# Kernel optimization log

Measured on AMD Instinct MI355X. Metric: run time of the kernel, lower is better.

## Reference

```python
import jax, jax.numpy as jnp
import numpy as np

B, N, XD = 64, 512, 32  # batch, n_points, x_dims (feature columns); last 2 cols are t, y


def setup_inputs() -> dict:
    key = jax.random.key(0)
    xtys = jax.random.normal(key, (B, N, XD + 2), dtype=jnp.float32)
    return {"xtys": xtys}


def _linear_dml(xtys):
    b, n, D = xtys.shape
    d = D - 2
    xs = xtys[..., :d]          # (b, n, d) covariates
    ts = xtys[..., d]           # (b, n)   treatment
    ys = xtys[..., d + 1]       # (b, n)   outcome

    # Growing-prefix least squares via cumulative sufficient statistics.
    # For prefix i (rows 0..i): min-norm lstsq solution w = pinv(X^T X) X^T v == pinv(X) v,
    # matching torch.linalg.lstsq (gelsy/gelsd) semantics including rank-deficient prefixes.
    G = jnp.cumsum(jnp.einsum('bnd,bne->bnde', xs, xs), axis=1)      # (b,n,d,d) Gram
    Xty = jnp.cumsum(xs * ys[..., None], axis=1)                     # (b,n,d)
    Xtt = jnp.cumsum(xs * ts[..., None], axis=1)                     # (b,n,d)
    Sty = jnp.cumsum(ts * ys, axis=1)                                # (b,n)
    Stt = jnp.cumsum(ts * ts, axis=1)                                # (b,n)

    Ginv = jnp.linalg.pinv(G)                                        # batched pinv, (b,n,d,d)
    wy = jnp.einsum('bnde,bne->bnd', Ginv, Xty)
    wt = jnp.einsum('bnde,bne->bnd', Ginv, Xtt)

    # ate_i = <t_res, y_res> / <t_res, t_res> over prefix, expanded via the stats above.
    num = (Sty
           - jnp.einsum('bnd,bnd->bn', wt, Xty)
           - jnp.einsum('bnd,bnd->bn', wy, Xtt)
           + jnp.einsum('bnd,bnde,bne->bn', wt, G, wy))
    den = (Stt
           - 2.0 * jnp.einsum('bnd,bnd->bn', wt, Xtt)
           + jnp.einsum('bnd,bnde,bne->bn', wt, G, wt))
    safe = den > 0
    ate = jnp.where(safe, num / jnp.where(safe, den, 1.0), 0.0)      # min-norm: 0 when thats==0

    means = ate.at[:, 0].set(0.0)                                    # i==0 special case
    stds = jnp.zeros_like(means)                                     # module always appends zeros
    return means, 2.0 * jnp.log(stds)                                # -> -inf, as in the original


def reference(xtys):
    return _linear_dml(xtys)
```

## Files before the change

### kernel.cpp

```cpp
#include <hip/hip_runtime.h>
#include <math.h>
#include <utility>

#define BB 64
#define NN 512
#define DD 32
#define ZD 34
#define NE 595
#define WIN 8
#define NW 64
#define WACT 60

#define SEG 4
#define RS 128
#define KWS 16
#define CH 4
#define ECH 149
#define PSTRIDE 17

#define SPW 5

using f2 = __attribute__((ext_vector_type(2))) float;

__device__ inline void ent2ij(int e, int& i, int& j) {
    int ii = 0, rem = e;
    while (rem >= ZD - ii) { rem -= (ZD - ii); ++ii; }
    i = ii; j = ii + rem;
}

template<int N> struct Pack { Pack<N - 1> head; float v; };
template<> struct Pack<1> { float v; };
template<int I, int N> __device__ __forceinline__ float& pget(Pack<N>& p) {
    static_assert(I < N, "oob");
    if constexpr (I == N - 1) return p.v;
    else return pget<I, N - 1>(p.head);
}

template<int N> struct PackP { PackP<N - 1> head; f2 v; };
template<> struct PackP<1> { f2 v; };
template<int I, int N> __device__ __forceinline__ f2& ppget(PackP<N>& p) {
    static_assert(I < N, "oob");
    if constexpr (I == N - 1) return p.v;
    else return ppget<I, N - 1>(p.head);
}
template<int R> __device__ __forceinline__ float prow(PackP<21>& p) {
    static_assert(R < 42, "oob");
    if constexpr (R & 1) return ppget<R / 2>(p).y;
    else                 return ppget<R / 2>(p).x;
}

__device__ __forceinline__ float rdlane(float x, int srclane) {
    return __int_as_float(__builtin_amdgcn_readlane(__float_as_int(x), srclane));
}
__device__ __forceinline__ float bperm(int byteaddr, float x) {
    return __int_as_float(__builtin_amdgcn_ds_bpermute(byteaddr, __float_as_int(x)));
}

__global__ __launch_bounds__(256) void dml_gram(const float* __restrict__ xtys,
                                                float* __restrict__ P,
                                                float* __restrict__ out) {
    const int t   = threadIdx.x;
    const int blk = blockIdx.x;
    const int c   = blk % CH;
    const int bg  = blk / CH;
    const int g   = bg % SEG;
    const int b   = bg / SEG;

    const int gid = blk * 256 + t;
    if (gid < BB * NN) out[BB * NN + gid] = 0.0f;
    if (gid < BB * DD) out[(gid >> 5) * NN + (gid & 31)] = 0.0f;

    __shared__ float zs[RS * ZD];
    const float* src = xtys + ((size_t)b * NN + (size_t)g * RS) * ZD;
    for (int u = t; u < RS * ZD; u += 256) zs[u] = src[u];
    __syncthreads();

    const int e = c * ECH + t;
    if (t < ECH && e < NE) {
        int i, j;
        ent2ij(e, i, j);
        float* pdst = P + (size_t)(b * SEG + g) * PSTRIDE * NE + e;
        double acc = 0.0;
#pragma unroll
        for (int k = 0; k < KWS; ++k) {
            pdst[k * NE] = (float)acc;
            double wsum = 0.0;
#pragma unroll
            for (int s8 = 0; s8 < WIN; ++s8) {
                const float* row = &zs[(k * WIN + s8) * ZD];
                wsum = fma((double)row[i], (double)row[j], wsum);
            }
            acc += wsum;
        }
        pdst[KWS * NE] = (float)acc;
    }
}


template<int R> __device__ __forceinline__
float initval(int j, int off_j, int zoff, const float* snL, const float* zb) {
    constexpr int RC = (R < DD) ? (R * ZD - (R * (R - 1)) / 2 - R) : 0;
    if constexpr (R < DD) {
        float v = 0.0f;
        if (j < DD) {
            int idx = (R < j) ? (RC + j) : (off_j + R);
            v = snL[idx];
        } else if (j < DD + WIN) {
            v = zb[zoff + R];
        } else if (j == 40) {
            v = snL[RC + DD];
        } else if (j == 41) {
            v = snL[RC + DD + 1];
        }
        return v;
    } else if constexpr (R < DD + WIN) {
        return (j < DD) ? zb[(R - DD) * ZD + j] : 0.0f;
    } else if constexpr (R == 40) {
        return (j < DD) ? snL[off_j + DD] : 0.0f;
    } else {
        return (j < DD) ? snL[off_j + DD + 1] : 0.0f;
    }
}
template<int P> __device__ __forceinline__
void init_rec(PackP<21>& A, int j, int off_j, int zoff,
              const float* snL, const float* zb) {
    if constexpr (P < 21) {
        f2 q;
        q.x = initval<2 * P>(j, off_j, zoff, snL, zb);
        q.y = initval<2 * P + 1>(j, off_j, zoff, snL, zb);
        ppget<P>(A) = q;
        init_rec<P + 1>(A, j, off_j, zoff, snL, zb);
    }
}

template<int K, int P> __device__ __forceinline__
void elim_pairs(PackP<21>& A, f2 t2) {
    if constexpr (P < 21) {
        f2 fr2;
        fr2.x = rdlane(prow<2 * P>(A), K);
        fr2.y = rdlane(prow<2 * P + 1>(A), K);
        ppget<P>(A) -= fr2 * t2;
        elim_pairs<K, P + 1>(A, t2);
    }
}
template<int K> __device__ __forceinline__
void elim_step(PackP<21>& A) {
    float piv  = rdlane(prow<K>(A), K);
    float invp = (piv > 1e-30f) ? 1.0f / piv : 0.0f;
    float t    = invp * prow<K>(A);
    f2 t2; t2.x = t; t2.y = t;
    elim_pairs<K, (K + 1) / 2>(A, t2);
}
template<int... Ks> __device__ __forceinline__
void elim_all(PackP<21>& A, std::integer_sequence<int, Ks...>) {
    ((elim_step<Ks>(A)), ...);
}

template<int R> __device__ __forceinline__
void kdump(PackP<21>& A, float* Kl, int c) {
    if constexpr (R < DD + 10) {
        if constexpr (R >= DD)
            Kl[(R - DD) * 10 + c] = -prow<R>(A);
        kdump<R + 1>(A, Kl, c);
    }
}

template<int L> __device__ __forceinline__
void tinit(Pack<12>& T, int row, int sys, const float* Kl, const float* zb) {
    if constexpr (L < 12) {
        float v;
        if constexpr (L < 8) {
            float kij = (row <= sys && L <= sys) ? Kl[row * 10 + L] : 0.0f;
            v = kij + ((row == L) ? 1.0f : 0.0f);
        } else if constexpr (L == 8)  v = (row <= sys) ? Kl[row * 10 + 8] : 0.0f;
        else if constexpr (L == 9)    v = (row <= sys) ? zb[row * ZD + DD] : 0.0f;
        else if constexpr (L == 10)   v = (row <= sys) ? Kl[row * 10 + 9] : 0.0f;
        else                          v = (row <= sys) ? zb[row * ZD + DD + 1] : 0.0f;
        pget<L>(T) = v;
        tinit<L + 1>(T, row, sys, Kl, zb);
    }
}
template<int K, int J> __device__ __forceinline__
void gjp_cols(Pack<12>& T, float f, int pb) {
    if constexpr (J < 12) {
        float pk = bperm(pb + 4 * K, pget<J>(T));
        pget<J>(T) = fmaf(-f, pk, pget<J>(T));
        gjp_cols<K, J + 1>(T, f, pb);
    }
}
template<int K> __device__ __forceinline__
void gjp_step(Pack<12>& T, int pb, int row, float& diag) {
    float pkK  = bperm(pb + 4 * K, pget<K>(T));
    float invp = (pkK > 1e-30f || pkK < -1e-30f) ? 1.0f / pkK : 0.0f;
    float f    = (row == K) ? 0.0f : pget<K>(T) * invp;
    gjp_cols<K, K + 1>(T, f, pb);
    if (row == K) diag = pget<K>(T);
}
template<int... Ks> __device__ __forceinline__
void gjp_all(Pack<12>& T, int pb, int row, float& diag,
             std::integer_sequence<int, Ks...>) {
    ((gjp_step<Ks>(T, pb, row, diag)), ...);
}

__global__ __launch_bounds__(320) void dml_solve(const float* __restrict__ xtys,
                                                 const float* __restrict__ P,
                                                 float* __restrict__ out) {
    const int wid  = threadIdx.x >> 6;
    const int lane = threadIdx.x & 63;
    const int id   = blockIdx.x * SPW + wid;
    const int w    = (id % WACT) + 4;
    const int b    = id / WACT;
    const int g    = w >> 4;
    const int k    = w & 15;

    __shared__ float snL[SPW][NE];
    __shared__ float zb[SPW][WIN * ZD];
    __shared__ float Kl[SPW][100];
    float* snW = snL[wid];
    float* zbW = zb[wid];
    float* KlW = Kl[wid];

    const float* pb_  = P + (size_t)b * SEG * PSTRIDE * NE;
    const float* src  = xtys + ((size_t)b * NN + (size_t)w * WIN) * ZD;
    for (int u = lane; u < NE; u += 64) {
        float v = pb_[(size_t)(g * PSTRIDE + k) * NE + u];
        for (int g2 = 0; g2 < g; ++g2)
            v += pb_[(size_t)(g2 * PSTRIDE + KWS) * NE + u];
        snW[u] = v;
    }
    for (int u = lane; u < WIN * ZD; u += 64) zbW[u] = src[u];

    const int j     = lane;
    const int off_j = j * (ZD - 1) - (j * (j - 1)) / 2;
    const int zoff  = (j - DD) * ZD;

    PackP<21> A;
    init_rec<0>(A, j, off_j, zoff, snW, zbW);

    elim_all(A, std::make_integer_sequence<int, DD>{});

    if (lane >= DD && lane < DD + 10) kdump<0>(A, KlW, lane - DD);

    const int sys = lane >> 3;
    const int row = lane & 7;
    const int pbB = (lane & ~7) << 2;

    Pack<12> T;
    tinit<0>(T, row, sys, KlW, zbW);
    float diag = 1.0f;
    gjp_all(T, pbB, row, diag, std::make_integer_sequence<int, 8>{});

    float dinv = (diag > 1e-30f || diag < -1e-30f) ? 1.0f / diag : 0.0f;
    double s1 = (double)(pget<8>(T) * dinv);
    double s2 = (double)(pget<9>(T) * dinv);
    double r1 = (double)(pget<10>(T) * dinv);
    double r2 = (double)(pget<11>(T) * dinv);
    double gg = (double)KlW[80 + row] - (double)zbW[row * ZD + DD];
    double cd = gg * (s1 - s2);
    double cn = gg * (r1 - r2);
#pragma unroll
    for (int m = 1; m < 8; m <<= 1) {
        cd += __shfl_xor(cd, m, 8);
        cn += __shfl_xor(cn, m, 8);
    }

    double Stt0 = (double)snW[592];
    double Sty0 = (double)snW[593];
    double den  = Stt0 - (double)KlW[88] + cd;
    double num  = Sty0 - (double)KlW[89] + cn;
    double val  = (den > 0.0) ? num / den : 0.0;
    if (!isfinite(val)) val = 0.0;
    if (row == 0) out[b * NN + w * WIN + sys] = (float)val;
}

extern "C" void kernel_launch(void* const* d_in, const int* in_sizes, int n_in,
                              void* d_out, int out_size, void* d_ws, size_t ws_size,
                              hipStream_t stream) {
    const float* xtys = (const float*)d_in[0];
    float* out = (float*)d_out;
    float* P = (float*)d_ws;

    hipLaunchKernelGGL(dml_gram, dim3(BB * SEG * CH), dim3(256), 0, stream, xtys, P, out);
    hipLaunchKernelGGL(dml_solve, dim3(BB * WACT / SPW), dim3(320), 0, stream, xtys, P, out);
}
```

Measured before the change: 93.22 us.

## Interleave two independent solve systems per wavefront for ILP

The solve kernel now runs one 64-thread wavefront per block, and each wavefront processes two window systems at once. The elimination and Gauss-Jordan steps are interleaved across the two register-resident matrices so their cross-lane reads and FMAs can overlap. This hides the latency of the serial dependent chain. In exchange it roughly doubles register pressure, which may cause spills or lower occupancy, and it halves the number of wavefronts launched.

```diff
diff --git a/kernel.cpp b/kernel.cpp
--- a/kernel.cpp
+++ b/kernel.cpp
@@ -17,8 +17,6 @@
 #define CH 4
 #define ECH 149
 #define PSTRIDE 17
-
-#define SPW 5
 
 using f2 = __attribute__((ext_vector_type(2))) float;
 
@@ -134,26 +132,33 @@
 }
 
 template<int K, int P> __device__ __forceinline__
-void elim_pairs(PackP<21>& A, f2 t2) {
+void elim_pairs2(PackP<21>& Aa, PackP<21>& Ab, f2 ta, f2 tb) {
     if constexpr (P < 21) {
-        f2 fr2;
-        fr2.x = rdlane(prow<2 * P>(A), K);
-        fr2.y = rdlane(prow<2 * P + 1>(A), K);
-        ppget<P>(A) -= fr2 * t2;
-        elim_pairs<K, P + 1>(A, t2);
+        f2 fa, fb;
+        fa.x = rdlane(prow<2 * P>(Aa), K);
+        fa.y = rdlane(prow<2 * P + 1>(Aa), K);
+        fb.x = rdlane(prow<2 * P>(Ab), K);
+        fb.y = rdlane(prow<2 * P + 1>(Ab), K);
+        ppget<P>(Aa) -= fa * ta;
+        ppget<P>(Ab) -= fb * tb;
+        elim_pairs2<K, P + 1>(Aa, Ab, ta, tb);
     }
 }
 template<int K> __device__ __forceinline__
-void elim_step(PackP<21>& A) {
-    float piv  = rdlane(prow<K>(A), K);
-    float invp = (piv > 1e-30f) ? 1.0f / piv : 0.0f;
-    float t    = invp * prow<K>(A);
-    f2 t2; t2.x = t; t2.y = t;
-    elim_pairs<K, (K + 1) / 2>(A, t2);
+void elim_step2(PackP<21>& Aa, PackP<21>& Ab) {
+    float pa = rdlane(prow<K>(Aa), K);
+    float pb = rdlane(prow<K>(Ab), K);
+    float ia = (pa > 1e-30f) ? 1.0f / pa : 0.0f;
+    float ib = (pb > 1e-30f) ? 1.0f / pb : 0.0f;
+    float ua = ia * prow<K>(Aa);
+    float ub = ib * prow<K>(Ab);
+    f2 ta; ta.x = ua; ta.y = ua;
+    f2 tb; tb.x = ub; tb.y = ub;
+    elim_pairs2<K, (K + 1) / 2>(Aa, Ab, ta, tb);
 }
 template<int... Ks> __device__ __forceinline__
-void elim_all(PackP<21>& A, std::integer_sequence<int, Ks...>) {
-    ((elim_step<Ks>(A)), ...);
+void elim_all2(PackP<21>& Aa, PackP<21>& Ab, std::integer_sequence<int, Ks...>) {
+    ((elim_step2<Ks>(Aa, Ab)), ...);
 }
 
 template<int R> __device__ __forceinline__
@@ -181,96 +186,124 @@
     }
 }
 template<int K, int J> __device__ __forceinline__
-void gjp_cols(Pack<12>& T, float f, int pb) {
+void gjp_cols2(Pack<12>& Ta, Pack<12>& Tb, float fa, float fb, int pb) {
     if constexpr (J < 12) {
-        float pk = bperm(pb + 4 * K, pget<J>(T));
-        pget<J>(T) = fmaf(-f, pk, pget<J>(T));
-        gjp_cols<K, J + 1>(T, f, pb);
+        float pka = bperm(pb + 4 * K, pget<J>(Ta));
+        float pkb = bperm(pb + 4 * K, pget<J>(Tb));
+        pget<J>(Ta) = fmaf(-fa, pka, pget<J>(Ta));
+        pget<J>(Tb) = fmaf(-fb, pkb, pget<J>(Tb));
+        gjp_cols2<K, J + 1>(Ta, Tb, fa, fb, pb);
     }
 }
 template<int K> __device__ __forceinline__
-void gjp_step(Pack<12>& T, int pb, int row, float& diag) {
-    float pkK  = bperm(pb + 4 * K, pget<K>(T));
-    float invp = (pkK > 1e-30f || pkK < -1e-30f) ? 1.0f / pkK : 0.0f;
-    float f    = (row == K) ? 0.0f : pget<K>(T) * invp;
-    gjp_cols<K, K + 1>(T, f, pb);
-    if (row == K) diag = pget<K>(T);
+void gjp_step2(Pack<12>& Ta, Pack<12>& Tb, int pb, int row,
+               float& diag_a, float& diag_b) {
+    float pka  = bperm(pb + 4 * K, pget<K>(Ta));
+    float pkb  = bperm(pb + 4 * K, pget<K>(Tb));
+    float ia   = (pka > 1e-30f || pka < -1e-30f) ? 1.0f / pka : 0.0f;
+    float ib   = (pkb > 1e-30f || pkb < -1e-30f) ? 1.0f / pkb : 0.0f;
+    float fa   = (row == K) ? 0.0f : pget<K>(Ta) * ia;
+    float fb   = (row == K) ? 0.0f : pget<K>(Tb) * ib;
+    gjp_cols2<K, K + 1>(Ta, Tb, fa, fb, pb);
+    if (row == K) { diag_a = pget<K>(Ta); diag_b = pget<K>(Tb); }
 }
 template<int... Ks> __device__ __forceinline__
-void gjp_all(Pack<12>& T, int pb, int row, float& diag,
-             std::integer_sequence<int, Ks...>) {
-    ((gjp_step<Ks>(T, pb, row, diag)), ...);
-}
-
-__global__ __launch_bounds__(320) void dml_solve(const float* __restrict__ xtys,
-                                                 const float* __restrict__ P,
-                                                 float* __restrict__ out) {
-    const int wid  = threadIdx.x >> 6;
-    const int lane = threadIdx.x & 63;
-    const int id   = blockIdx.x * SPW + wid;
-    const int w    = (id % WACT) + 4;
-    const int b    = id / WACT;
-    const int g    = w >> 4;
-    const int k    = w & 15;
-
-    __shared__ float snL[SPW][NE];
-    __shared__ float zb[SPW][WIN * ZD];
-    __shared__ float Kl[SPW][100];
-    float* snW = snL[wid];
-    float* zbW = zb[wid];
-    float* KlW = Kl[wid];
-
-    const float* pb_  = P + (size_t)b * SEG * PSTRIDE * NE;
-    const float* src  = xtys + ((size_t)b * NN + (size_t)w * WIN) * ZD;
+void gjp_all2(Pack<12>& Ta, Pack<12>& Tb, int pb, int row,
+              float& diag_a, float& diag_b, std::integer_sequence<int, Ks...>) {
+    ((gjp_step2<Ks>(Ta, Tb, pb, row, diag_a, diag_b)), ...);
+}
+
+__global__ __launch_bounds__(64) void dml_solve(const float* __restrict__ xtys,
+                                                const float* __restrict__ P,
+                                                float* __restrict__ out) {
+    const int lane = threadIdx.x;
+    const int ida  = blockIdx.x * 2;
+    const int idb  = ida + 1;
+    const int wa   = (ida % WACT) + 4;
+    const int ba   = ida / WACT;
+    const int wb   = (idb % WACT) + 4;
+    const int bb   = idb / WACT;
+    const int ga   = wa >> 4, ka = wa & 15;
+    const int gb   = wb >> 4, kb = wb & 15;
+
+    __shared__ float snL[2][NE];
+    __shared__ float zbS[2][WIN * ZD];
+    __shared__ float KlS[2][100];
+
+    const float* pba  = P + (size_t)ba * SEG * PSTRIDE * NE;
+    const float* pbb  = P + (size_t)bb * SEG * PSTRIDE * NE;
+    const float* sra  = xtys + ((size_t)ba * NN + (size_t)wa * WIN) * ZD;
+    const float* srb  = xtys + ((size_t)bb * NN + (size_t)wb * WIN) * ZD;
     for (int u = lane; u < NE; u += 64) {
-        float v = pb_[(size_t)(g * PSTRIDE + k) * NE + u];
-        for (int g2 = 0; g2 < g; ++g2)
-            v += pb_[(size_t)(g2 * PSTRIDE + KWS) * NE + u];
-        snW[u] = v;
-    }
-    for (int u = lane; u < WIN * ZD; u += 64) zbW[u] = src[u];
+        float va = pba[(size_t)(ga * PSTRIDE + ka) * NE + u];
+        float vb = pbb[(size_t)(gb * PSTRIDE + kb) * NE + u];
+        for (int g2 = 0; g2 < ga; ++g2)
+            va += pba[(size_t)(g2 * PSTRIDE + KWS) * NE + u];
+        for (int g2 = 0; g2 < gb; ++g2)
+            vb += pbb[(size_t)(g2 * PSTRIDE + KWS) * NE + u];
+        snL[0][u] = va;
+        snL[1][u] = vb;
+    }
+    for (int u = lane; u < WIN * ZD; u += 64) {
+        zbS[0][u] = sra[u];
+        zbS[1][u] = srb[u];
+    }
 
     const int j     = lane;
     const int off_j = j * (ZD - 1) - (j * (j - 1)) / 2;
     const int zoff  = (j - DD) * ZD;
 
-    PackP<21> A;
-    init_rec<0>(A, j, off_j, zoff, snW, zbW);
-
-    elim_all(A, std::make_integer_sequence<int, DD>{});
-
-    if (lane >= DD && lane < DD + 10) kdump<0>(A, KlW, lane - DD);
+    PackP<21> Aa, Ab;
+    init_rec<0>(Aa, j, off_j, zoff, snL[0], zbS[0]);
+    init_rec<0>(Ab, j, off_j, zoff, snL[1], zbS[1]);
+
+    elim_all2(Aa, Ab, std::make_integer_sequence<int, DD>{});
+
+    if (lane >= DD && lane < DD + 10) {
+        kdump<0>(Aa, KlS[0], lane - DD);
+        kdump<0>(Ab, KlS[1], lane - DD);
+    }
 
     const int sys = lane >> 3;
     const int row = lane & 7;
     const int pbB = (lane & ~7) << 2;
 
-    Pack<12> T;
-    tinit<0>(T, row, sys, KlW, zbW);
-    float diag = 1.0f;
-    gjp_all(T, pbB, row, diag, std::make_integer_sequence<int, 8>{});
-
-    float dinv = (diag > 1e-30f || diag < -1e-30f) ? 1.0f / diag : 0.0f;
-    double s1 = (double)(pget<8>(T) * dinv);
-    double s2 = (double)(pget<9>(T) * dinv);
-    double r1 = (double)(pget<10>(T) * dinv);
-    double r2 = (double)(pget<11>(T) * dinv);
-    double gg = (double)KlW[80 + row] - (double)zbW[row * ZD + DD];
-    double cd = gg * (s1 - s2);
-    double cn = gg * (r1 - r2);
+    Pack<12> Ta, Tb;
+    tinit<0>(Ta, row, sys, KlS[0], zbS[0]);
+    tinit<0>(Tb, row, sys, KlS[1], zbS[1]);
+    float diag_a = 1.0f, diag_b = 1.0f;
+    gjp_all2(Ta, Tb, pbB, row, diag_a, diag_b, std::make_integer_sequence<int, 8>{});
+
+    float dia = (diag_a > 1e-30f || diag_a < -1e-30f) ? 1.0f / diag_a : 0.0f;
+    float dib = (diag_b > 1e-30f || diag_b < -1e-30f) ? 1.0f / diag_b : 0.0f;
+    double s1a = (double)(pget<8>(Ta) * dia),  s1b = (double)(pget<8>(Tb) * dib);
+    double s2a = (double)(pget<9>(Ta) * dia),  s2b = (double)(pget<9>(Tb) * dib);
+    double r1a = (double)(pget<10>(Ta) * dia), r1b = (double)(pget<10>(Tb) * dib);
+    double r2a = (double)(pget<11>(Ta) * dia), r2b = (double)(pget<11>(Tb) * dib);
+    double gga = (double)KlS[0][80 + row] - (double)zbS[0][row * ZD + DD];
+    double ggb = (double)KlS[1][80 + row] - (double)zbS[1][row * ZD + DD];
+    double cda = gga * (s1a - s2a), cdb = ggb * (s1b - s2b);
+    double cna = gga * (r1a - r2a), cnb = ggb * (r1b - r2b);
 #pragma unroll
     for (int m = 1; m < 8; m <<= 1) {
-        cd += __shfl_xor(cd, m, 8);
-        cn += __shfl_xor(cn, m, 8);
-    }
-
-    double Stt0 = (double)snW[592];
-    double Sty0 = (double)snW[593];
-    double den  = Stt0 - (double)KlW[88] + cd;
-    double num  = Sty0 - (double)KlW[89] + cn;
-    double val  = (den > 0.0) ? num / den : 0.0;
-    if (!isfinite(val)) val = 0.0;
-    if (row == 0) out[b * NN + w * WIN + sys] = (float)val;
+        cda += __shfl_xor(cda, m, 8);
+        cna += __shfl_xor(cna, m, 8);
+        cdb += __shfl_xor(cdb, m, 8);
+        cnb += __shfl_xor(cnb, m, 8);
+    }
+
+    double dena = (double)snL[0][592] - (double)KlS[0][88] + cda;
+    double numa = (double)snL[0][593] - (double)KlS[0][89] + cna;
+    double denb = (double)snL[1][592] - (double)KlS[1][88] + cdb;
+    double numb = (double)snL[1][593] - (double)KlS[1][89] + cnb;
+    double vala = (dena > 0.0) ? numa / dena : 0.0;
+    double valb = (denb > 0.0) ? numb / denb : 0.0;
+    if (!isfinite(vala)) vala = 0.0;
+    if (!isfinite(valb)) valb = 0.0;
+    if (row == 0) {
+        out[ba * NN + wa * WIN + sys] = (float)vala;
+        out[bb * NN + wb * WIN + sys] = (float)valb;
+    }
 }
 
 extern "C" void kernel_launch(void* const* d_in, const int* in_sizes, int n_in,
@@ -281,5 +314,5 @@
     float* P = (float*)d_ws;
 
     hipLaunchKernelGGL(dml_gram, dim3(BB * SEG * CH), dim3(256), 0, stream, xtys, P, out);
-    hipLaunchKernelGGL(dml_solve, dim3(BB * WACT / SPW), dim3(320), 0, stream, xtys, P, out);
-}
+    hipLaunchKernelGGL(dml_solve, dim3(BB * WACT / 2), dim3(64), 0, stream, xtys, P, out);
+}
```

Result: slower. 106.2 us (+13.9%).
